# Kernel tuning notes

Hardware: AMD Instinct MI355X
Metric: run time of the kernel (lower is better)

## Reference

```python
import jax, jax.numpy as jnp
import numpy as np

B, L, D, H = 8, 1024, 1024, 16
DPH = D // H  # 64


def setup_inputs() -> dict:
    key = jax.random.key(0)
    ks = jax.random.split(key, 12)
    s = 1.0 / np.sqrt(D)
    return {
        "key": jax.random.normal(ks[0], (B, L, D), jnp.float32),
        "value": jax.random.normal(ks[1], (B, L, D), jnp.float32),
        "query": jax.random.normal(ks[2], (B, L, D), jnp.float32),
        "attn_mask": jax.random.randint(ks[3], (B, L, L), 0, 2) > 0,
        "Wq": jax.random.normal(ks[4], (D, D), jnp.float32) * s,
        "bq": jnp.zeros((D,), jnp.float32),
        "Wk": jax.random.normal(ks[5], (D, D), jnp.float32) * s,
        "bk": jnp.zeros((D,), jnp.float32),
        "Wv": jax.random.normal(ks[6], (D, D), jnp.float32) * s,
        "bv": jnp.zeros((D,), jnp.float32),
        "Wo": jax.random.normal(ks[7], (D, D), jnp.float32) * s,
        "bo": jnp.zeros((D,), jnp.float32),
        "gamma": jnp.ones((D,), jnp.float32),
        "beta": jnp.zeros((D,), jnp.float32),
    }


def _layer_norm(x, gamma, beta, eps=1e-5):
    mu = jnp.mean(x, axis=-1, keepdims=True)
    var = jnp.var(x, axis=-1, keepdims=True)
    return (x - mu) * jax.lax.rsqrt(var + eps) * gamma + beta


def reference(key, value, query, attn_mask, Wq, bq, Wk, bk, Wv, bv, Wo, bo, gamma, beta):
    residual = query
    k = key @ Wk + bk      # [B, L, D]
    v = value @ Wv + bv
    q = query @ Wq + bq
    # faithful to torch: raw row-major view into [B*H, L, dph] (NOT standard head transpose)
    k = k.reshape(B * H, -1, DPH)
    v = v.reshape(B * H, -1, DPH)
    q = q.reshape(B * H, -1, DPH)
    # faithful to torch repeat: tile whole batch H times along dim 0
    mask = jnp.tile(attn_mask, (H, 1, 1))  # [B*H, L, L]
    scale = DPH ** (-0.5)
    scores = jnp.einsum('bqd,bkd->bqk', q, k) * scale
    scores = jnp.where(mask, jnp.float32(-1e9), scores)
    attention = jax.nn.softmax(scores, axis=2)
    context = jnp.einsum('bqk,bkd->bqd', attention, v)  # [B*H, L, dph]
    context = context.reshape(B, -1, D)
    output = context @ Wo + bo
    output = _layer_norm(residual + output, gamma, beta)
    return (output, attention)
```

## Files before the change

kernel.cpp:

```cpp
#include <hip/hip_runtime.h>

typedef __attribute__((ext_vector_type(8))) short short8;
typedef __attribute__((ext_vector_type(4))) float f32x4;

#define AS1C(p) ((const __attribute__((address_space(1))) void*)(p))
#define AS3(p)  ((__attribute__((address_space(3))) void*)(p))

__device__ __forceinline__ unsigned short f2bf(float f) {
  unsigned int u = __float_as_uint(f);
  return (unsigned short)((u + 0x7fffu + ((u >> 16) & 1u)) >> 16);
}

__device__ __forceinline__ void gload16(const void* g, void* l) {
  __builtin_amdgcn_global_load_lds(AS1C(g), AS3(l), 16, 0, 0);
}

#define EXP_C 0.18033688011112042f

__global__ __launch_bounds__(256) void conv3_bf16(const float* __restrict__ s0,
                                                  const float* __restrict__ s1,
                                                  const float* __restrict__ s2,
                                                  unsigned short* __restrict__ d0,
                                                  unsigned short* __restrict__ d1,
                                                  unsigned short* __restrict__ d2, int n4) {
  const float* in = (blockIdx.z == 0) ? s0 : (blockIdx.z == 1) ? s1 : s2;
  unsigned short* out = (blockIdx.z == 0) ? d0 : (blockIdx.z == 1) ? d1 : d2;
  int i = blockIdx.x * 256 + threadIdx.x;
  if (i >= n4) return;
  float4 v = ((const float4*)in)[i];
  ushort4 o;
  o.x = f2bf(v.x); o.y = f2bf(v.y); o.z = f2bf(v.z); o.w = f2bf(v.w);
  ((ushort4*)out)[i] = o;
}

__global__ __launch_bounds__(256) void pack_mask_kernel(const int* __restrict__ m,
                                                        unsigned int* __restrict__ bits) {
  int i = blockIdx.x * 256 + threadIdx.x;
  unsigned long long bl = __ballot(m[i] != 0);
  if ((threadIdx.x & 63) == 0) {
    bits[(i >> 5)]     = (unsigned int)bl;
    bits[(i >> 5) + 1] = (unsigned int)(bl >> 32);
  }
}

__global__ __launch_bounds__(256) void transpose_w(const float* __restrict__ W0,
                                                   const float* __restrict__ W1,
                                                   const float* __restrict__ W2,
                                                   const float* __restrict__ W3,
                                                   unsigned short* __restrict__ WtBase) {
  __shared__ float t[32][33];
  const float* W = (blockIdx.z == 0) ? W0 : (blockIdx.z == 1) ? W1 : (blockIdx.z == 2) ? W2 : W3;
  unsigned short* Wt = WtBase + (size_t)blockIdx.z * 1024 * 1024;
  int bx = blockIdx.x * 32, by = blockIdx.y * 32;
  int tx = threadIdx.x & 31, ty = threadIdx.x >> 5;
#pragma unroll
  for (int i = 0; i < 4; ++i) {
    int r = ty + i * 8;
    t[r][tx] = W[(size_t)(by + r) * 1024 + bx + tx];
  }
  __syncthreads();
#pragma unroll
  for (int i = 0; i < 4; ++i) {
    int r = ty + i * 8;
    Wt[(size_t)(bx + r) * 1024 + by + tx] = f2bf(t[tx][r]);
  }
}

__global__ __launch_bounds__(256) void transpose_v(const unsigned short* __restrict__ v,
                                                   unsigned short* __restrict__ vt) {
  __shared__ unsigned short t[32][33];
  int b = blockIdx.z;
  int bx = blockIdx.x * 32;
  int by = blockIdx.y * 32;
  int tx = threadIdx.x & 31, ty = threadIdx.x >> 5;
#pragma unroll
  for (int i = 0; i < 4; ++i) {
    int r = ty + i * 8;
    t[r][tx] = v[(size_t)b * 65536 + (size_t)(by + r) * 64 + bx + tx];
  }
  __syncthreads();
#pragma unroll
  for (int i = 0; i < 4; ++i) {
    int r = ty + i * 8;
    vt[(size_t)b * 65536 + (size_t)(bx + r) * 1024 + by + tx] = t[tx][r];
  }
}

template <int MODE>
__device__ __forceinline__ void gemm_body(
    const unsigned short* __restrict__ A, const unsigned short* __restrict__ Bt,
    const float* __restrict__ bias, const float* __restrict__ res,
    unsigned short* __restrict__ Cb, float* __restrict__ Cf,
    unsigned short* lA, unsigned short* lB) {
  const int K = 1024, N = 1024;
  const int tid = threadIdx.x;
  const int wave = tid >> 6, lane = tid & 63;
  const int row_l = lane & 15, kg = lane >> 4;
  const int wg = blockIdx.y * 8 + blockIdx.x;
  const int idx = (wg & 7) * 64 + (wg >> 3);
  const int m0 = (idx >> 3) * 128, n0 = (idx & 7) * 128;
  const int wm = (wave >> 1) * 64, wn = (wave & 1) * 64;
  f32x4 acc[4][4] = {};

  for (int k0 = 0; k0 < K; k0 += 32) {
    __syncthreads();
#pragma unroll
    for (int it = 0; it < 2; ++it) {
      int c = wave * 64 + it * 256 + lane;
      int r = c >> 2, ch = c & 3;
      int sch = ch ^ (r & 3);
      gload16(A + (size_t)(m0 + r) * K + k0 + sch * 8, lA + (wave * 64 + it * 256) * 8);
      gload16(Bt + (size_t)(n0 + r) * K + k0 + sch * 8, lB + (wave * 64 + it * 256) * 8);
    }
    __syncthreads();
    short8 af[4], bfr[4];
#pragma unroll
    for (int t = 0; t < 4; ++t) {
      int ra = wm + t * 16 + row_l;
      af[t] = *(const short8*)(lA + ra * 32 + ((kg ^ (ra & 3)) << 3));
      int rb = wn + t * 16 + row_l;
      bfr[t] = *(const short8*)(lB + rb * 32 + ((kg ^ (rb & 3)) << 3));
    }
    __builtin_amdgcn_s_setprio(1);
#pragma unroll
    for (int mt = 0; mt < 4; ++mt)
#pragma unroll
      for (int nt = 0; nt < 4; ++nt)
        acc[mt][nt] = __builtin_amdgcn_mfma_f32_16x16x32_bf16(af[mt], bfr[nt], acc[mt][nt], 0, 0, 0);
    __builtin_amdgcn_s_setprio(0);
  }
#pragma unroll
  for (int mt = 0; mt < 4; ++mt)
#pragma unroll
    for (int nt = 0; nt < 4; ++nt)
#pragma unroll
      for (int r = 0; r < 4; ++r) {
        int grow = m0 + wm + mt * 16 + kg * 4 + r;
        int gcol = n0 + wn + nt * 16 + row_l;
        float v = acc[mt][nt][r] + bias[gcol];
        if (MODE == 0) {
          Cb[(size_t)grow * N + gcol] = f2bf(v);
        } else {
          v += res[(size_t)grow * N + gcol];
          Cf[(size_t)grow * N + gcol] = v;
        }
      }
}

__global__ __launch_bounds__(256) void gemm_qk_kernel(
    const unsigned short* __restrict__ A0, const unsigned short* __restrict__ A1,
    const unsigned short* __restrict__ WtBase,
    const float* __restrict__ b0, const float* __restrict__ b1,
    unsigned short* __restrict__ C0, unsigned short* __restrict__ C1) {
  __shared__ unsigned short lA[128 * 32];
  __shared__ unsigned short lB[128 * 32];
  int z = blockIdx.z;
  const unsigned short* A = (z == 0) ? A0 : A1;
  const float* bias = (z == 0) ? b0 : b1;
  unsigned short* C = (z == 0) ? C0 : C1;
  gemm_body<0>(A, WtBase + (size_t)z * 1024 * 1024, bias, nullptr, C, nullptr, lA, lB);
}

__global__ __launch_bounds__(256) void gemm_proj_kernel(
    const unsigned short* __restrict__ A, const unsigned short* __restrict__ Bt,
    const float* __restrict__ bias, unsigned short* __restrict__ Cb) {
  __shared__ unsigned short lA[128 * 32];
  __shared__ unsigned short lB[128 * 32];
  gemm_body<0>(A, Bt, bias, nullptr, Cb, nullptr, lA, lB);
}

__global__ __launch_bounds__(256) void gemm_out_kernel(
    const unsigned short* __restrict__ A, const unsigned short* __restrict__ Bt,
    const float* __restrict__ bias, const float* __restrict__ res, float* __restrict__ Cf) {
  __shared__ unsigned short lA[128 * 32];
  __shared__ unsigned short lB[128 * 32];
  gemm_body<1>(A, Bt, bias, res, nullptr, Cf, lA, lB);
}

__global__ __launch_bounds__(256) void attn_kernel(
    const unsigned short* __restrict__ Q,
    const unsigned short* __restrict__ Km,
    const unsigned short* __restrict__ Vt,
    const unsigned int* __restrict__ mbits,
    float* __restrict__ attn,
    unsigned short* __restrict__ ctx) {
  __shared__ unsigned short lQ[64 * 64];
  __shared__ unsigned short lK[64 * 64];
  __shared__ unsigned short lV[64 * 64];
  const int tid = threadIdx.x, wave = tid >> 6, lane = tid & 63;
  const int row_l = lane & 15, kg = lane >> 4;
  const int wg = blockIdx.y * 16 + blockIdx.x;
  const int idx = (wg & 7) * 256 + (wg >> 3);
  const int batch = idx >> 4, qt = idx & 15;
  const int q0 = qt * 64;
  const unsigned short* Qb = Q + (size_t)batch * 65536;
  const unsigned short* Kb = Km + (size_t)batch * 65536;
  const unsigned short* Vb = Vt + (size_t)batch * 65536;
  const unsigned int* mrow = mbits + (size_t)(batch & 7) * 32768;
  float* attb = attn + (size_t)batch * 1048576;
  const int qrow_base = q0 + wave * 16 + kg * 4;

#define STAGE_K_TO(kt, dst)                                                           \
  {                                                                                   \
    _Pragma("unroll") for (int it = 0; it < 2; ++it) {                                \
      int c = wave * 64 + it * 256 + lane;                                            \
      int r_ = c >> 3, ch_ = c & 7, sch_ = ch_ ^ (r_ & 7);                            \
      gload16(Kb + (size_t)((kt) * 64 + r_) * 64 + sch_ * 8,                          \
              (dst) + (wave * 64 + it * 256) * 8);                                    \
    }                                                                                 \
  }
#define STAGE_V_TO(kt, dst)                                                           \
  {                                                                                   \
    _Pragma("unroll") for (int it = 0; it < 2; ++it) {                                \
      int c = wave * 64 + it * 256 + lane;                                            \
      int r_ = c >> 3, ch_ = c & 7, sch_ = ch_ ^ (r_ & 7);                            \
      gload16(Vb + (size_t)r_ * 1024 + (kt) * 64 + sch_ * 8,                          \
              (dst) + (wave * 64 + it * 256) * 8);                                    \
    }                                                                                 \
  }
#define WAIT_BAR0                                             \
  asm volatile("s_waitcnt vmcnt(0)" ::: "memory");            \
  __builtin_amdgcn_s_barrier();

#pragma unroll
  for (int it = 0; it < 2; ++it) {
    int c = wave * 64 + it * 256 + lane;
    int r = c >> 3, ch = c & 7;
    int sch = ch ^ (r & 7);
    gload16(Qb + (size_t)(q0 + r) * 64 + sch * 8, lQ + (wave * 64 + it * 256) * 8);
  }
  STAGE_K_TO(0, lK)
  WAIT_BAR0
  short8 qf[2];
  {
    int rq = wave * 16 + row_l;
#pragma unroll
    for (int kk = 0; kk < 2; ++kk)
      qf[kk] = *(const short8*)(lQ + rq * 64 + (((kk * 4 + kg) ^ (rq & 7)) << 3));
  }

  float l_part[4] = {0.f, 0.f, 0.f, 0.f};

  auto pass1_step = [&](const unsigned short* kbuf, int kt) {
    f32x4 s[4];
    __builtin_amdgcn_s_setprio(1);
#pragma unroll
    for (int cf = 0; cf < 4; ++cf) {
      int rk = cf * 16 + row_l;
      f32x4 a = {0.f, 0.f, 0.f, 0.f};
#pragma unroll
      for (int kk = 0; kk < 2; ++kk) {
        short8 kf = *(const short8*)(kbuf + rk * 64 + (((kk * 4 + kg) ^ (rk & 7)) << 3));
        a = __builtin_amdgcn_mfma_f32_16x16x32_bf16(qf[kk], kf, a, 0, 0, 0);
      }
      s[cf] = a;
    }
    __builtin_amdgcn_s_setprio(0);
#pragma unroll
    for (int r = 0; r < 4; ++r) {
      unsigned int w0 = mrow[(qrow_base + r) * 32 + kt * 2];
      unsigned int w1 = mrow[(qrow_base + r) * 32 + kt * 2 + 1];
#pragma unroll
      for (int cf = 0; cf < 4; ++cf) {
        int kl = cf * 16 + row_l;
        unsigned int w = (kl & 32) ? w1 : w0;
        int bit = (w >> (kl & 31)) & 1;
        float e = __builtin_exp2f(s[cf][r] * EXP_C);
        l_part[r] += bit ? 0.f : e;
      }
    }
  };
  for (int kt2 = 0; kt2 < 16; kt2 += 2) {
    STAGE_K_TO(kt2 + 1, lV)
    pass1_step(lK, kt2);
    WAIT_BAR0
    if (kt2 + 2 < 16) STAGE_K_TO(kt2 + 2, lK)
    pass1_step(lV, kt2 + 1);
    WAIT_BAR0
  }
  float il[4];
#pragma unroll
  for (int r = 0; r < 4; ++r) {
    float se = l_part[r];
#pragma unroll
    for (int sh = 1; sh < 16; sh <<= 1) se += __shfl_xor(se, sh);
    il[r] = 1.f / se;
  }

  f32x4 cacc[4] = {};
  unsigned short* lP = lQ;

  for (int kt = 0; kt < 16; ++kt) {
    __syncthreads();
    STAGE_K_TO(kt, lK)
    STAGE_V_TO(kt, lV)
    WAIT_BAR0
    f32x4 s[4];
    __builtin_amdgcn_s_setprio(1);
#pragma unroll
    for (int cf = 0; cf < 4; ++cf) {
      int rk = cf * 16 + row_l;
      f32x4 a = {0.f, 0.f, 0.f, 0.f};
#pragma unroll
      for (int kk = 0; kk < 2; ++kk) {
        short8 kf = *(const short8*)(lK + rk * 64 + (((kk * 4 + kg) ^ (rk & 7)) << 3));
        a = __builtin_amdgcn_mfma_f32_16x16x32_bf16(qf[kk], kf, a, 0, 0, 0);
      }
      s[cf] = a;
    }
    __builtin_amdgcn_s_setprio(0);
#pragma unroll
    for (int r = 0; r < 4; ++r) {
      unsigned int w0 = mrow[(qrow_base + r) * 32 + kt * 2];
      unsigned int w1 = mrow[(qrow_base + r) * 32 + kt * 2 + 1];
      float* arow = attb + (size_t)(qrow_base + r) * 1024 + kt * 64;
      int prow = wave * 16 + kg * 4 + r;
#pragma unroll
      for (int cf = 0; cf < 4; ++cf) {
        int kl = cf * 16 + row_l;
        unsigned int w = (kl & 32) ? w1 : w0;
        int bit = (w >> (kl & 31)) & 1;
        float e = __builtin_exp2f(s[cf][r] * EXP_C) * il[r];
        float p = bit ? 0.f : e;
        __builtin_nontemporal_store(p, arow + kl);
        int pch = (kl >> 3) ^ (prow & 7);
        lP[prow * 64 + pch * 8 + (kl & 7)] = f2bf(p);
      }
    }
    __builtin_amdgcn_s_setprio(1);
#pragma unroll
    for (int kk = 0; kk < 2; ++kk) {
      int rp = wave * 16 + row_l;
      short8 pa = *(const short8*)(lP + rp * 64 + (((kk * 4 + kg) ^ (rp & 7)) << 3));
#pragma unroll
      for (int df = 0; df < 4; ++df) {
        int rv = df * 16 + row_l;
        short8 vb = *(const short8*)(lV + rv * 64 + (((kk * 4 + kg) ^ (rv & 7)) << 3));
        cacc[df] = __builtin_amdgcn_mfma_f32_16x16x32_bf16(pa, vb, cacc[df], 0, 0, 0);
      }
    }
    __builtin_amdgcn_s_setprio(0);
  }
#pragma unroll
  for (int df = 0; df < 4; ++df)
#pragma unroll
    for (int r = 0; r < 4; ++r) {
      int grow = q0 + wave * 16 + kg * 4 + r;
      int gcol = df * 16 + row_l;
      ctx[(size_t)batch * 65536 + (size_t)grow * 64 + gcol] = f2bf(cacc[df][r]);
    }
#undef STAGE_K_TO
#undef STAGE_V_TO
#undef WAIT_BAR0
}

__global__ __launch_bounds__(256) void layernorm_kernel(float* __restrict__ io,
                                                        const float* __restrict__ gamma,
                                                        const float* __restrict__ beta) {
  int wave = threadIdx.x >> 6, lane = threadIdx.x & 63;
  size_t row = (size_t)blockIdx.x * 4 + wave;
  float* p = io + row * 1024;
  float4 v[4];
  float s = 0.f, ss = 0.f;
#pragma unroll
  for (int i = 0; i < 4; ++i) {
    v[i] = ((const float4*)p)[lane + i * 64];
    s += v[i].x + v[i].y + v[i].z + v[i].w;
    ss += v[i].x * v[i].x + v[i].y * v[i].y + v[i].z * v[i].z + v[i].w * v[i].w;
  }
#pragma unroll
  for (int m = 1; m < 64; m <<= 1) { s += __shfl_xor(s, m); ss += __shfl_xor(ss, m); }
  float mu = s * (1.f / 1024.f);
  float var = ss * (1.f / 1024.f) - mu * mu;
  float rinv = rsqrtf(var + 1e-5f);
#pragma unroll
  for (int i = 0; i < 4; ++i) {
    int idx = lane + i * 64;
    float4 g = ((const float4*)gamma)[idx];
    float4 b = ((const float4*)beta)[idx];
    float4 o;
    o.x = (v[i].x - mu) * rinv * g.x + b.x;
    o.y = (v[i].y - mu) * rinv * g.y + b.y;
    o.z = (v[i].z - mu) * rinv * g.z + b.z;
    o.w = (v[i].w - mu) * rinv * g.w + b.w;
    ((float4*)p)[idx] = o;
  }
}

extern "C" void kernel_launch(void* const* d_in, const int* in_sizes, int n_in,
                              void* d_out, int out_size, void* d_ws, size_t ws_size,
                              hipStream_t stream) {
  const float* key   = (const float*)d_in[0];
  const float* value = (const float*)d_in[1];
  const float* query = (const float*)d_in[2];
  const int* amask   = (const int*)d_in[3];
  const float* Wq = (const float*)d_in[4];
  const float* bq = (const float*)d_in[5];
  const float* Wk = (const float*)d_in[6];
  const float* bk = (const float*)d_in[7];
  const float* Wv = (const float*)d_in[8];
  const float* bv = (const float*)d_in[9];
  const float* Wo = (const float*)d_in[10];
  const float* bo = (const float*)d_in[11];
  const float* gamma = (const float*)d_in[12];
  const float* beta  = (const float*)d_in[13];

  char* ws = (char*)d_ws;
  const size_t MB = 1024 * 1024;
  float* out_f = (float*)d_out;
  float* attn_f = (float*)d_out + (size_t)8388608;
  const int n4 = 8388608 / 4;
  dim3 gemm_grid(8, 64);
  dim3 gemm_grid2(8, 64, 2);
  dim3 attn_grid(16, 128);

  const bool big_ws = ws_size >= 106 * MB;
  if (big_ws) {
    unsigned short* A0 = (unsigned short*)(ws + 0);
    unsigned short* A1 = (unsigned short*)(ws + 16 * MB);
    unsigned short* A2 = (unsigned short*)(ws + 32 * MB);
    unsigned short* B1 = (unsigned short*)(ws + 48 * MB);
    unsigned short* B2 = (unsigned short*)(ws + 64 * MB);
    unsigned short* B3 = (unsigned short*)(ws + 80 * MB);
    unsigned short* Wts = (unsigned short*)(ws + 96 * MB);
    unsigned int* mbits = (unsigned int*)(ws + 104 * MB);

    transpose_w<<<dim3(32, 32, 4), 256, 0, stream>>>(Wq, Wk, Wv, Wo, Wts);
    pack_mask_kernel<<<32768, 256, 0, stream>>>(amask, mbits);
    conv3_bf16<<<dim3(8192, 1, 3), 256, 0, stream>>>(query, key, value, A0, A1, A2, n4);
    gemm_qk_kernel<<<gemm_grid2, 256, 0, stream>>>(A0, A1, Wts, bq, bk, B1, B2);
    gemm_proj_kernel<<<gemm_grid, 256, 0, stream>>>(A2, Wts + 2 * MB, bv, B3);
    transpose_v<<<dim3(2, 32, 128), 256, 0, stream>>>(B3, A1);
    attn_kernel<<<attn_grid, 256, 0, stream>>>(B1, B2, A1, mbits, attn_f, A2);
    gemm_out_kernel<<<gemm_grid, 256, 0, stream>>>(A2, Wts + 3 * MB, bo, query, out_f);
    layernorm_kernel<<<2048, 256, 0, stream>>>(out_f, gamma, beta);
  } else {
    unsigned short* B0 = (unsigned short*)(ws + 0);
    unsigned short* B1 = (unsigned short*)(ws + 16 * MB);
    unsigned short* B2 = (unsigned short*)(ws + 32 * MB);
    unsigned short* B3 = (unsigned short*)(ws + 48 * MB);
    unsigned short* Wts = (unsigned short*)(ws + 64 * MB);
    unsigned int* mbits = (unsigned int*)(ws + 72 * MB);

    transpose_w<<<dim3(32, 32, 4), 256, 0, stream>>>(Wq, Wk, Wv, Wo, Wts);
    pack_mask_kernel<<<32768, 256, 0, stream>>>(amask, mbits);
    conv3_bf16<<<dim3(8192, 1, 1), 256, 0, stream>>>(query, query, query, B0, B0, B0, n4);
    gemm_qk_kernel<<<gemm_grid, 256, 0, stream>>>(B0, B0, Wts, bq, bq, B1, B1);
    conv3_bf16<<<dim3(8192, 1, 1), 256, 0, stream>>>(key, key, key, B0, B0, B0, n4);
    gemm_qk_kernel<<<gemm_grid, 256, 0, stream>>>(B0, B0, Wts + 1 * MB, bk, bk, B2, B2);
    conv3_bf16<<<dim3(8192, 1, 1), 256, 0, stream>>>(value, value, value, B0, B0, B0, n4);
    gemm_proj_kernel<<<gemm_grid, 256, 0, stream>>>(B0, Wts + 2 * MB, bv, B3);
    transpose_v<<<dim3(2, 32, 128), 256, 0, stream>>>(B3, B0);
    attn_kernel<<<attn_grid, 256, 0, stream>>>(B1, B2, B0, mbits, attn_f, B3);
    gemm_out_kernel<<<gemm_grid, 256, 0, stream>>>(B3, Wts + 3 * MB, bo, query, out_f);
    layernorm_kernel<<<2048, 256, 0, stream>>>(out_f, gamma, beta);
  }
}
```

Baseline: 359.9 us.

## Swap MFMA operands so lanes own query rows; transpose packed mask bits

Swaps the A/B operands of the QK^T MFMA so each lane holds one query row and four consecutive key columns. This lets the attention-probability output be written as 16-byte float4 stores instead of scalar nontemporal stores, and the bf16 P tile go to LDS as 8-byte stores. The packed mask is stored transposed (word index major, query minor), so each lane loads two coalesced mask words per tile instead of eight scattered ones. The row-sum reduction shrinks to two cross-lane shuffles. The nontemporal hint on the large attention write is dropped, and the mask-packing writes become strided.

After: 413.2 us. +14.8%, slower.

```diff
diff --git a/kernel.cpp b/kernel.cpp
--- a/kernel.cpp
+++ b/kernel.cpp
@@ -34,12 +34,14 @@
 }
 
 __global__ __launch_bounds__(256) void pack_mask_kernel(const int* __restrict__ m,
-                                                        unsigned int* __restrict__ bits) {
+                                                        unsigned int* __restrict__ bitsT) {
   int i = blockIdx.x * 256 + threadIdx.x;
   unsigned long long bl = __ballot(m[i] != 0);
   if ((threadIdx.x & 63) == 0) {
-    bits[(i >> 5)]     = (unsigned int)bl;
-    bits[(i >> 5) + 1] = (unsigned int)(bl >> 32);
+    int b_ = i >> 20, q = (i >> 10) & 1023, k = i & 1023;
+    int w = k >> 5;
+    bitsT[b_ * 32768 + w * 1024 + q]       = (unsigned int)bl;
+    bitsT[b_ * 32768 + (w + 1) * 1024 + q] = (unsigned int)(bl >> 32);
   }
 }
 
@@ -181,7 +183,7 @@
     const unsigned short* __restrict__ Q,
     const unsigned short* __restrict__ Km,
     const unsigned short* __restrict__ Vt,
-    const unsigned int* __restrict__ mbits,
+    const unsigned int* __restrict__ mbitsT,
     float* __restrict__ attn,
     unsigned short* __restrict__ ctx) {
   __shared__ unsigned short lQ[64 * 64];
@@ -196,9 +198,10 @@
   const unsigned short* Qb = Q + (size_t)batch * 65536;
   const unsigned short* Kb = Km + (size_t)batch * 65536;
   const unsigned short* Vb = Vt + (size_t)batch * 65536;
-  const unsigned int* mrow = mbits + (size_t)(batch & 7) * 32768;
+  const unsigned int* mT = mbitsT + (size_t)(batch & 7) * 32768;
   float* attb = attn + (size_t)batch * 1048576;
-  const int qrow_base = q0 + wave * 16 + kg * 4;
+  const int q_loc = wave * 16 + row_l;
+  const int q_lane = q0 + q_loc;
 
 #define STAGE_K_TO(kt, dst)                                                           \
   {                                                                                   \
@@ -232,16 +235,15 @@
   STAGE_K_TO(0, lK)
   WAIT_BAR0
   short8 qf[2];
-  {
-    int rq = wave * 16 + row_l;
-#pragma unroll
-    for (int kk = 0; kk < 2; ++kk)
-      qf[kk] = *(const short8*)(lQ + rq * 64 + (((kk * 4 + kg) ^ (rq & 7)) << 3));
-  }
-
-  float l_part[4] = {0.f, 0.f, 0.f, 0.f};
+#pragma unroll
+  for (int kk = 0; kk < 2; ++kk)
+    qf[kk] = *(const short8*)(lQ + q_loc * 64 + (((kk * 4 + kg) ^ (q_loc & 7)) << 3));
+
+  float l_part = 0.f;
 
   auto pass1_step = [&](const unsigned short* kbuf, int kt) {
+    unsigned int mw0 = mT[(kt * 2 + 0) * 1024 + q_lane];
+    unsigned int mw1 = mT[(kt * 2 + 1) * 1024 + q_lane];
     f32x4 s[4];
     __builtin_amdgcn_s_setprio(1);
 #pragma unroll
@@ -251,22 +253,19 @@
 #pragma unroll
       for (int kk = 0; kk < 2; ++kk) {
         short8 kf = *(const short8*)(kbuf + rk * 64 + (((kk * 4 + kg) ^ (rk & 7)) << 3));
-        a = __builtin_amdgcn_mfma_f32_16x16x32_bf16(qf[kk], kf, a, 0, 0, 0);
+        a = __builtin_amdgcn_mfma_f32_16x16x32_bf16(kf, qf[kk], a, 0, 0, 0);
       }
       s[cf] = a;
     }
     __builtin_amdgcn_s_setprio(0);
 #pragma unroll
-    for (int r = 0; r < 4; ++r) {
-      unsigned int w0 = mrow[(qrow_base + r) * 32 + kt * 2];
-      unsigned int w1 = mrow[(qrow_base + r) * 32 + kt * 2 + 1];
-#pragma unroll
-      for (int cf = 0; cf < 4; ++cf) {
-        int kl = cf * 16 + row_l;
-        unsigned int w = (kl & 32) ? w1 : w0;
-        int bit = (w >> (kl & 31)) & 1;
+    for (int cf = 0; cf < 4; ++cf) {
+      unsigned int w = (cf < 2) ? mw0 : mw1;
+#pragma unroll
+      for (int r = 0; r < 4; ++r) {
+        int bit = (w >> ((cf & 1) * 16 + kg * 4 + r)) & 1;
         float e = __builtin_exp2f(s[cf][r] * EXP_C);
-        l_part[r] += bit ? 0.f : e;
+        l_part += bit ? 0.f : e;
       }
     }
   };
@@ -278,14 +277,10 @@
     pass1_step(lV, kt2 + 1);
     WAIT_BAR0
   }
-  float il[4];
-#pragma unroll
-  for (int r = 0; r < 4; ++r) {
-    float se = l_part[r];
-#pragma unroll
-    for (int sh = 1; sh < 16; sh <<= 1) se += __shfl_xor(se, sh);
-    il[r] = 1.f / se;
-  }
+  float se = l_part;
+  se += __shfl_xor(se, 16);
+  se += __shfl_xor(se, 32);
+  const float il = 1.f / se;
 
   f32x4 cacc[4] = {};
   unsigned short* lP = lQ;
@@ -295,6 +290,8 @@
     STAGE_K_TO(kt, lK)
     STAGE_V_TO(kt, lV)
     WAIT_BAR0
+    unsigned int mw0 = mT[(kt * 2 + 0) * 1024 + q_lane];
+    unsigned int mw1 = mT[(kt * 2 + 1) * 1024 + q_lane];
     f32x4 s[4];
     __builtin_amdgcn_s_setprio(1);
 #pragma unroll
@@ -304,34 +301,31 @@
 #pragma unroll
       for (int kk = 0; kk < 2; ++kk) {
         short8 kf = *(const short8*)(lK + rk * 64 + (((kk * 4 + kg) ^ (rk & 7)) << 3));
-        a = __builtin_amdgcn_mfma_f32_16x16x32_bf16(qf[kk], kf, a, 0, 0, 0);
+        a = __builtin_amdgcn_mfma_f32_16x16x32_bf16(kf, qf[kk], a, 0, 0, 0);
       }
       s[cf] = a;
     }
     __builtin_amdgcn_s_setprio(0);
 #pragma unroll
-    for (int r = 0; r < 4; ++r) {
-      unsigned int w0 = mrow[(qrow_base + r) * 32 + kt * 2];
-      unsigned int w1 = mrow[(qrow_base + r) * 32 + kt * 2 + 1];
-      float* arow = attb + (size_t)(qrow_base + r) * 1024 + kt * 64;
-      int prow = wave * 16 + kg * 4 + r;
-#pragma unroll
-      for (int cf = 0; cf < 4; ++cf) {
-        int kl = cf * 16 + row_l;
-        unsigned int w = (kl & 32) ? w1 : w0;
-        int bit = (w >> (kl & 31)) & 1;
-        float e = __builtin_exp2f(s[cf][r] * EXP_C) * il[r];
-        float p = bit ? 0.f : e;
-        __builtin_nontemporal_store(p, arow + kl);
-        int pch = (kl >> 3) ^ (prow & 7);
-        lP[prow * 64 + pch * 8 + (kl & 7)] = f2bf(p);
-      }
+    for (int cf = 0; cf < 4; ++cf) {
+      unsigned int w = (cf < 2) ? mw0 : mw1;
+      f32x4 o;
+      unsigned short pb[4];
+#pragma unroll
+      for (int r = 0; r < 4; ++r) {
+        int bit = (w >> ((cf & 1) * 16 + kg * 4 + r)) & 1;
+        float p = bit ? 0.f : __builtin_exp2f(s[cf][r] * EXP_C) * il;
+        o[r] = p;
+        pb[r] = f2bf(p);
+      }
+      int swc = (cf * 2 + (kg >> 1)) ^ (q_loc & 7);
+      *(uint2*)((char*)lP + q_loc * 128 + swc * 16 + (kg & 1) * 8) = *(const uint2*)pb;
+      *(f32x4*)(attb + (size_t)q_lane * 1024 + kt * 64 + cf * 16 + kg * 4) = o;
     }
     __builtin_amdgcn_s_setprio(1);
 #pragma unroll
     for (int kk = 0; kk < 2; ++kk) {
-      int rp = wave * 16 + row_l;
-      short8 pa = *(const short8*)(lP + rp * 64 + (((kk * 4 + kg) ^ (rp & 7)) << 3));
+      short8 pa = *(const short8*)(lP + q_loc * 64 + (((kk * 4 + kg) ^ (q_loc & 7)) << 3));
 #pragma unroll
       for (int df = 0; df < 4; ++df) {
         int rv = df * 16 + row_l;
@@ -423,15 +417,15 @@
     unsigned short* B2 = (unsigned short*)(ws + 64 * MB);
     unsigned short* B3 = (unsigned short*)(ws + 80 * MB);
     unsigned short* Wts = (unsigned short*)(ws + 96 * MB);
-    unsigned int* mbits = (unsigned int*)(ws + 104 * MB);
+    unsigned int* mbitsT = (unsigned int*)(ws + 104 * MB);
 
     transpose_w<<<dim3(32, 32, 4), 256, 0, stream>>>(Wq, Wk, Wv, Wo, Wts);
-    pack_mask_kernel<<<32768, 256, 0, stream>>>(amask, mbits);
+    pack_mask_kernel<<<32768, 256, 0, stream>>>(amask, mbitsT);
     conv3_bf16<<<dim3(8192, 1, 3), 256, 0, stream>>>(query, key, value, A0, A1, A2, n4);
     gemm_qk_kernel<<<gemm_grid2, 256, 0, stream>>>(A0, A1, Wts, bq, bk, B1, B2);
     gemm_proj_kernel<<<gemm_grid, 256, 0, stream>>>(A2, Wts + 2 * MB, bv, B3);
     transpose_v<<<dim3(2, 32, 128), 256, 0, stream>>>(B3, A1);
-    attn_kernel<<<attn_grid, 256, 0, stream>>>(B1, B2, A1, mbits, attn_f, A2);
+    attn_kernel<<<attn_grid, 256, 0, stream>>>(B1, B2, A1, mbitsT, attn_f, A2);
     gemm_out_kernel<<<gemm_grid, 256, 0, stream>>>(A2, Wts + 3 * MB, bo, query, out_f);
     layernorm_kernel<<<2048, 256, 0, stream>>>(out_f, gamma, beta);
   } else {
@@ -440,10 +434,10 @@
     unsigned short* B2 = (unsigned short*)(ws + 32 * MB);
     unsigned short* B3 = (unsigned short*)(ws + 48 * MB);
     unsigned short* Wts = (unsigned short*)(ws + 64 * MB);
-    unsigned int* mbits = (unsigned int*)(ws + 72 * MB);
+    unsigned int* mbitsT = (unsigned int*)(ws + 72 * MB);
 
     transpose_w<<<dim3(32, 32, 4), 256, 0, stream>>>(Wq, Wk, Wv, Wo, Wts);
-    pack_mask_kernel<<<32768, 256, 0, stream>>>(amask, mbits);
+    pack_mask_kernel<<<32768, 256, 0, stream>>>(amask, mbitsT);
     conv3_bf16<<<dim3(8192, 1, 1), 256, 0, stream>>>(query, query, query, B0, B0, B0, n4);
     gemm_qk_kernel<<<gemm_grid, 256, 0, stream>>>(B0, B0, Wts, bq, bq, B1, B1);
     conv3_bf16<<<dim3(8192, 1, 1), 256, 0, stream>>>(key, key, key, B0, B0, B0, n4);
@@ -451,7 +445,7 @@
     conv3_bf16<<<dim3(8192, 1, 1), 256, 0, stream>>>(value, value, value, B0, B0, B0, n4);
     gemm_proj_kernel<<<gemm_grid, 256, 0, stream>>>(B0, Wts + 2 * MB, bv, B3);
     transpose_v<<<dim3(2, 32, 128), 256, 0, stream>>>(B3, B0);
-    attn_kernel<<<attn_grid, 256, 0, stream>>>(B1, B2, B0, mbits, attn_f, B3);
+    attn_kernel<<<attn_grid, 256, 0, stream>>>(B1, B2, B0, mbitsT, attn_f, B3);
     gemm_out_kernel<<<gemm_grid, 256, 0, stream>>>(B3, Wts + 3 * MB, bo, query, out_f);
     layernorm_kernel<<<2048, 256, 0, stream>>>(out_f, gamma, beta);
   }
```
